# Kernel optimization log

Hardware: AMD Instinct MI355X
Metric: run time of the kernel (lower is better)

Reference implementation:

```python
import jax, jax.numpy as jnp
import numpy as np

N, C_IN, C_OUT, HID, HEADS, K = 8192, 256, 256, 256, 4, 16
DH = HID // HEADS
EPS = 1e-12


def _safe_norm(v, axis=-1):
    return jnp.sqrt(jnp.sum(v * v, axis=axis) + EPS)


def _angle(u, v):
    # angle(u, v) = atan2(||u x v||, u . v)  (standard PPF angle)
    cross = jnp.cross(u, v)
    return jnp.arctan2(_safe_norm(cross), jnp.sum(u * v, axis=-1))


def setup_inputs() -> dict:
    key = jax.random.key(0)
    ks = jax.random.split(key, 12)
    w = lambda k, sh, fan: (jax.random.normal(k, sh, jnp.float32) / np.sqrt(fan)).astype(jnp.float32)
    return {
        'p': jax.random.uniform(ks[0], (N, 3), jnp.float32),
        'normals': jax.random.normal(ks[1], (N, 3), jnp.float32),
        'x': jax.random.normal(ks[2], (N, C_IN), jnp.float32),
        'Wq': w(ks[3], (C_IN, HID), C_IN), 'bq': jnp.zeros((HID,), jnp.float32),
        'Wk': w(ks[4], (C_IN, HID), C_IN), 'bk': jnp.zeros((HID,), jnp.float32),
        'Wv': w(ks[5], (C_IN, HID), C_IN), 'bv': jnp.zeros((HID,), jnp.float32),
        'Wp1': w(ks[6], (4, HID), 4), 'bp1': jnp.zeros((HID,), jnp.float32),
        'Wp2': w(ks[7], (HID, HID), HID), 'bp2': jnp.zeros((HID,), jnp.float32),
        'Wo': w(ks[8], (HID, C_OUT), HID), 'bo': jnp.zeros((C_OUT,), jnp.float32),
    }


def reference(p, normals, x, Wq, bq, Wk, bk, Wv, bv, Wp1, bp1, Wp2, bp2, Wo, bo):
    normals = normals / _safe_norm(normals)[:, None]
    # --- kNN grouping (queryandgroup, stride==1: queries == support) ---
    sq = jnp.sum(p * p, axis=-1)                      # [N]
    d2 = sq[:, None] + sq[None, :] - 2.0 * (p @ p.T)  # [N, N]
    _, group_idx = jax.lax.top_k(-d2, K)              # [N, K] nearest (incl. self)
    c_p = p[group_idx]        # [N, K, 3]
    c_n = normals[group_idx]  # [N, K, 3]
    # --- PPF features (calc_ppf_gpu) ---
    vec_d = c_p - p[:, None, :]                       # [N, K, 3]
    dist = _safe_norm(vec_d)                          # [N, K]
    n1 = jnp.broadcast_to(normals[:, None, :], c_n.shape)
    ppf = jnp.stack([_angle(n1, vec_d), _angle(c_n, vec_d), _angle(n1, c_n), dist], axis=-1)  # [N, K, 4]
    # --- Local PPF transformer: grouped multi-head attention with PPF pos-enc ---
    q = (x @ Wq + bq).reshape(N, HEADS, DH)           # [N, H, Dh]
    feats = x[group_idx]                              # [N, K, C_IN]
    pe = jax.nn.relu(ppf @ Wp1 + bp1) @ Wp2 + bp2     # [N, K, HID]
    kf = (feats @ Wk + bk + pe).reshape(N, K, HEADS, DH)
    vf = (feats @ Wv + bv + pe).reshape(N, K, HEADS, DH)
    logits = jnp.einsum('nhd,nkhd->nhk', q, kf) / np.sqrt(DH)
    attn = jax.nn.softmax(logits, axis=-1)            # [N, H, K]
    out = jnp.einsum('nhk,nkhd->nhd', attn, vf).reshape(N, HID)
    return out @ Wo + bo                              # [N, C_OUT]
```

## Files before the change

### kernel.cpp

```cpp
#include <hip/hip_runtime.h>
#include <math.h>
#include <float.h>

#define NPTS 8192
#define CIN 256
#define HIDN 256
#define KNN 16

typedef unsigned short ushort_t;
typedef unsigned int uint_t;

__device__ __forceinline__ ushort_t f2b(float f) {
  uint_t u = __float_as_uint(f);
  u += 0x7fff + ((u >> 16) & 1);
  return (ushort_t)(u >> 16);
}
__device__ __forceinline__ float b2f(ushort_t s) {
  return __uint_as_float(((uint_t)s) << 16);
}

__global__ __launch_bounds__(256) void prep_kernel(const float* __restrict__ p,
                                                   const float* __restrict__ nr,
                                                   float* __restrict__ sq,
                                                   float* __restrict__ un) {
  int i = blockIdx.x * blockDim.x + threadIdx.x;
  if (i >= NPTS) return;
  float x = p[3*i+0], y = p[3*i+1], z = p[3*i+2];
  sq[i] = x*x + y*y + z*z;
  float a = nr[3*i+0], b = nr[3*i+1], c = nr[3*i+2];
  float nrm = sqrtf(a*a + b*b + c*c + 1e-12f);
  un[3*i+0] = a / nrm;
  un[3*i+1] = b / nrm;
  un[3*i+2] = c / nrm;
}

__device__ __forceinline__ bool dless(float d1, int i1, float d2, int i2) {
  return (d1 < d2) || (d1 == d2 && i1 < i2);
}

__global__ __launch_bounds__(256) void knn_kernel(const float* __restrict__ p,
                                                  const float* __restrict__ sq,
                                                  int* __restrict__ gidx) {
  const int wave = threadIdx.x >> 6;
  const int lane = threadIdx.x & 63;
  const int n = blockIdx.x * 4 + wave;
  const float px = p[3*n+0], py = p[3*n+1], pz = p[3*n+2];
  const float sn = sq[n];
  float d[KNN]; int id[KNN];
#pragma unroll
  for (int i = 0; i < KNN; ++i) { d[i] = FLT_MAX; id[i] = 0x7fffffff; }

  for (int c = 0; c < NPTS/64; ++c) {
    int j = c*64 + lane;
    float ax = p[3*j+0], ay = p[3*j+1], az = p[3*j+2];
    float dot = px*ax + py*ay + pz*az;
    float d2 = sn + sq[j] - 2.0f*dot;
    if (dless(d2, j, d[KNN-1], id[KNN-1])) {
      float cd = d2; int cj = j;
#pragma unroll
      for (int i = 0; i < KNN; ++i) {
        bool b = dless(cd, cj, d[i], id[i]);
        float td = d[i]; int tj = id[i];
        d[i]  = b ? cd : td;  id[i] = b ? cj : tj;
        cd    = b ? td : cd;  cj    = b ? tj : cj;
      }
    }
  }
  for (int r = 0; r < KNN; ++r) {
    float md = d[0]; int mj = id[0];
#pragma unroll
    for (int s = 1; s < 64; s <<= 1) {
      float od = __shfl_xor(md, s);
      int   oj = __shfl_xor(mj, s);
      if (dless(od, oj, md, mj)) { md = od; mj = oj; }
    }
    if (d[0] == md && id[0] == mj) {
#pragma unroll
      for (int i = 0; i < KNN-1; ++i) { d[i] = d[i+1]; id[i] = id[i+1]; }
      d[KNN-1] = FLT_MAX; id[KNN-1] = 0x7fffffff;
    }
    if (lane == 0) gidx[n*KNN + r] = mj;
  }
}

__global__ __launch_bounds__(128) void tile_gemm_kernel(const float* __restrict__ A,
                                                        const float* __restrict__ W,
                                                        const float* __restrict__ bias,
                                                        float* __restrict__ out) {
  __shared__ float At[16][36];
  __shared__ float Bs[16][132];
  const int t = threadIdx.x;
  const int row0 = blockIdx.x * 32;
  const int col0 = blockIdx.y * 128;
  const int tr = t & 7;
  const int tc = t >> 3;
  float acc[4][8];
#pragma unroll
  for (int i = 0; i < 4; ++i)
#pragma unroll
    for (int j = 0; j < 8; ++j) acc[i][j] = 0.f;

  for (int kt = 0; kt < 16; ++kt) {
    __syncthreads();
    {
      const int kk = t & 15, rb = t >> 4;
#pragma unroll
      for (int i = 0; i < 4; ++i) {
        int r = rb*4 + i;
        At[kk][r] = A[(size_t)(row0 + r)*256 + kt*16 + kk];
      }
#pragma unroll
      for (int k = 0; k < 16; ++k)
        Bs[k][t] = W[(size_t)(kt*16 + k)*256 + col0 + t];
    }
    __syncthreads();
#pragma unroll
    for (int k = 0; k < 16; ++k) {
      float4 a4 = *(const float4*)&At[k][tr*4];
      float4 b0 = *(const float4*)&Bs[k][tc*8];
      float4 b1 = *(const float4*)&Bs[k][tc*8 + 4];
      float av[4] = {a4.x, a4.y, a4.z, a4.w};
      float bv[8] = {b0.x, b0.y, b0.z, b0.w, b1.x, b1.y, b1.z, b1.w};
#pragma unroll
      for (int i = 0; i < 4; ++i)
#pragma unroll
        for (int j = 0; j < 8; ++j) acc[i][j] = fmaf(av[i], bv[j], acc[i][j]);
    }
  }
  float4 bb0 = *(const float4*)(bias + col0 + tc*8);
  float4 bb1 = *(const float4*)(bias + col0 + tc*8 + 4);
  float bv[8] = {bb0.x, bb0.y, bb0.z, bb0.w, bb1.x, bb1.y, bb1.z, bb1.w};
#pragma unroll
  for (int i = 0; i < 4; ++i) {
    int row = row0 + tr*4 + i;
    float4 o0, o1;
    o0.x = acc[i][0]+bv[0]; o0.y = acc[i][1]+bv[1]; o0.z = acc[i][2]+bv[2]; o0.w = acc[i][3]+bv[3];
    o1.x = acc[i][4]+bv[4]; o1.y = acc[i][5]+bv[5]; o1.z = acc[i][6]+bv[6]; o1.w = acc[i][7]+bv[7];
    *(float4*)(out + (size_t)row*256 + col0 + tc*8)     = o0;
    *(float4*)(out + (size_t)row*256 + col0 + tc*8 + 4) = o1;
  }
}

__global__ __launch_bounds__(256) void gemmG_kernel(const float* __restrict__ qx,
                                                    const float* __restrict__ Wp2,
                                                    uint_t* __restrict__ G) {
  __shared__ float At[16][68];
  __shared__ float Bs[16][260];
  const int t = threadIdx.x;
  const int row0 = blockIdx.x * 64;
  const int h = blockIdx.y;
  const int tr = t & 15;
  const int tc = t >> 4;
  float acc[4][16];
#pragma unroll
  for (int i = 0; i < 4; ++i)
#pragma unroll
    for (int j = 0; j < 16; ++j) acc[i][j] = 0.f;

  for (int kt = 0; kt < 4; ++kt) {
    __syncthreads();
    {
      const int kk = t & 15, rb = t >> 4;
#pragma unroll
      for (int i = 0; i < 4; ++i) {
        int r = rb*4 + i;
        At[kk][r] = qx[(size_t)(row0 + r)*256 + h*64 + kt*16 + kk];
      }
      const float* src = Wp2 + (size_t)t*256 + h*64 + kt*16;
#pragma unroll
      for (int q = 0; q < 4; ++q) {
        float4 v = *(const float4*)(src + q*4);
        Bs[q*4+0][t] = v.x;
        Bs[q*4+1][t] = v.y;
        Bs[q*4+2][t] = v.z;
        Bs[q*4+3][t] = v.w;
      }
    }
    __syncthreads();
#pragma unroll
    for (int k = 0; k < 16; ++k) {
      float4 a4 = *(const float4*)&At[k][tr*4];
      float av[4] = {a4.x, a4.y, a4.z, a4.w};
#pragma unroll
      for (int q = 0; q < 4; ++q) {
        float4 b4 = *(const float4*)&Bs[k][tc*16 + q*4];
        float bvv[4] = {b4.x, b4.y, b4.z, b4.w};
#pragma unroll
        for (int i = 0; i < 4; ++i)
#pragma unroll
          for (int e = 0; e < 4; ++e)
            acc[i][q*4+e] = fmaf(av[i], bvv[e], acc[i][q*4+e]);
      }
    }
  }
#pragma unroll
  for (int i = 0; i < 4; ++i) {
    int row = row0 + tr*4 + i;
#pragma unroll
    for (int j2 = 0; j2 < 8; ++j2) {
      uint_t pack = ((uint_t)f2b(acc[i][j2*2+1]) << 16) | (uint_t)f2b(acc[i][j2*2]);
      G[(size_t)row*512 + h*128 + tc*8 + j2] = pack;
    }
  }
}

__device__ __forceinline__ float angle3(float ux, float uy, float uz,
                                        float vx, float vy, float vz) {
  float cx = uy*vz - uz*vy;
  float cy = uz*vx - ux*vz;
  float cz = ux*vy - uy*vx;
  float cn = sqrtf(cx*cx + cy*cy + cz*cz + 1e-12f);
  float d  = ux*vx + uy*vy + uz*vz;
  return atan2f(cn, d);
}

__global__ __launch_bounds__(128) void fused_attn2_kernel(
    const float* __restrict__ p, const float* __restrict__ un,
    const int* __restrict__ gidx,
    const float* __restrict__ Wp1, const float* __restrict__ bp1,
    const float* __restrict__ bp2,
    const float* __restrict__ qx, const float* __restrict__ kx,
    const float* __restrict__ vx,
    const ushort_t* __restrict__ G, ushort_t* __restrict__ hbar,
    float* __restrict__ att) {
  __shared__ int   gid_s[KNN];
  __shared__ float ppf_s[KNN][4];
  __shared__ float h1_s[KNN][260];
  __shared__ float G_s[1024];
  __shared__ float q_s[256];
  __shared__ float w_s[64];
  const int n = blockIdx.x;
  const int t = threadIdx.x;

  if (t < KNN) gid_s[t] = gidx[n*KNN + t];
  q_s[t]       = qx[(size_t)n*256 + t];
  q_s[t + 128] = qx[(size_t)n*256 + t + 128];
  {
    const uint_t* gp = (const uint_t*)(G + (size_t)n*1024) + t*4;
#pragma unroll
    for (int q = 0; q < 4; ++q) {
      uint_t raw = gp[q];
      G_s[t*8 + q*2]     = __uint_as_float(raw << 16);
      G_s[t*8 + q*2 + 1] = __uint_as_float(raw & 0xffff0000u);
    }
  }
  __syncthreads();
  if (t < KNN) {
    int g = gid_s[t];
    float dx = p[3*g+0] - p[3*n+0];
    float dy = p[3*g+1] - p[3*n+1];
    float dz = p[3*g+2] - p[3*n+2];
    float n1x = un[3*n+0], n1y = un[3*n+1], n1z = un[3*n+2];
    float n2x = un[3*g+0], n2y = un[3*g+1], n2z = un[3*g+2];
    ppf_s[t][0] = angle3(n1x,n1y,n1z, dx,dy,dz);
    ppf_s[t][1] = angle3(n2x,n2y,n2z, dx,dy,dz);
    ppf_s[t][2] = angle3(n1x,n1y,n1z, n2x,n2y,n2z);
    ppf_s[t][3] = sqrtf(dx*dx + dy*dy + dz*dz + 1e-12f);
  }
  __syncthreads();

  {
    float w0[4], w1[4];
#pragma unroll
    for (int c = 0; c < 4; ++c) {
      w0[c] = Wp1[c*256 + t];
      w1[c] = Wp1[c*256 + t + 128];
    }
    float b0 = bp1[t], b1 = bp1[t+128];
#pragma unroll
    for (int k = 0; k < KNN; ++k) {
      float a0 = ppf_s[k][0], a1 = ppf_s[k][1], a2 = ppf_s[k][2], a3 = ppf_s[k][3];
      float s0 = b0 + a0*w0[0] + a1*w0[1] + a2*w0[2] + a3*w0[3];
      float s1 = b1 + a0*w1[0] + a1*w1[1] + a2*w1[2] + a3*w1[3];
      h1_s[k][t]     = fmaxf(s0, 0.f);
      h1_s[k][t+128] = fmaxf(s1, 0.f);
    }
  }
  __syncthreads();

  {
    const int pr = t >> 1;
    const int h  = pr >> 4;
    const int k  = pr & 15;
    const int half = t & 1;
    const int g = gid_s[k];
    float s = 0.f;
    const float* Gh = G_s + h*256 + half*128;
    const float* H  = &h1_s[k][half*128];
#pragma unroll 8
    for (int j4 = 0; j4 < 32; ++j4) {
      float4 gv = *(const float4*)(Gh + j4*4);
      float4 hv = *(const float4*)(H + j4*4);
      s = fmaf(gv.x, hv.x, s); s = fmaf(gv.y, hv.y, s);
      s = fmaf(gv.z, hv.z, s); s = fmaf(gv.w, hv.w, s);
    }
    const float* qh = q_s + h*64 + half*32;
    const float* kr = kx + (size_t)g*256 + h*64 + half*32;
#pragma unroll
    for (int c4 = 0; c4 < 8; ++c4) {
      float4 qv = *(const float4*)(qh + c4*4);
      float4 kv = *(const float4*)(kr + c4*4);
      s = fmaf(qv.x, kv.x, s); s = fmaf(qv.y, kv.y, s);
      s = fmaf(qv.z, kv.z, s); s = fmaf(qv.w, kv.w, s);
    }
    s += __shfl_xor(s, 1);
    float logit = s * 0.125f;
    float m = logit;
    m = fmaxf(m, __shfl_xor(m, 2));
    m = fmaxf(m, __shfl_xor(m, 4));
    m = fmaxf(m, __shfl_xor(m, 8));
    m = fmaxf(m, __shfl_xor(m, 16));
    float e = expf(logit - m);
    float sum = e;
    sum += __shfl_xor(sum, 2);
    sum += __shfl_xor(sum, 4);
    sum += __shfl_xor(sum, 8);
    sum += __shfl_xor(sum, 16);
    float w = e / sum;
    if (half == 0) w_s[pr] = w;
  }
  __syncthreads();

  {
    float hb0[4] = {0,0,0,0}, hb1[4] = {0,0,0,0};
#pragma unroll
    for (int kk = 0; kk < KNN; ++kk) {
      float h1v0 = h1_s[kk][t];
      float h1v1 = h1_s[kk][t+128];
#pragma unroll
      for (int hh = 0; hh < 4; ++hh) {
        float wv = w_s[hh*16 + kk];
        hb0[hh] = fmaf(wv, h1v0, hb0[hh]);
        hb1[hh] = fmaf(wv, h1v1, hb1[hh]);
      }
    }
#pragma unroll
    for (int hh = 0; hh < 4; ++hh) {
      hbar[(size_t)n*1024 + hh*256 + t]       = f2b(hb0[hh]);
      hbar[(size_t)n*1024 + hh*256 + t + 128] = f2b(hb1[hh]);
    }
  }

  {
    const int h0 = t >> 6;
    const int h1i = 2 + (t >> 6);
    float o0 = bp2[t], o1 = bp2[t+128];
#pragma unroll
    for (int kk = 0; kk < KNN; ++kk) {
      int gg = gid_s[kk];
      float w0v = w_s[h0*16 + kk];
      float w1v = w_s[h1i*16 + kk];
      o0 = fmaf(w0v, vx[(size_t)gg*256 + t], o0);
      o1 = fmaf(w1v, vx[(size_t)gg*256 + t + 128], o1);
    }
    att[(size_t)n*256 + t]       = o0;
    att[(size_t)n*256 + t + 128] = o1;
  }
}

__global__ __launch_bounds__(64) void gemm2_kernel(const ushort_t* __restrict__ hbar,
                                                   const float* __restrict__ Wp2,
                                                   float* __restrict__ att) {
  __shared__ float At[16][68];
  __shared__ float Bs[16][68];
  const int t = threadIdx.x;
  const int row0 = blockIdx.x * 64;
  const int h = blockIdx.y;
  const int tr = t & 7;
  const int tc = t >> 3;
  float acc[8][8];
#pragma unroll
  for (int i = 0; i < 8; ++i)
#pragma unroll
    for (int j = 0; j < 8; ++j) acc[i][j] = 0.f;

  for (int kt = 0; kt < 16; ++kt) {
    __syncthreads();
    {
      const int kk = t & 15, rb = t >> 4;
#pragma unroll
      for (int i = 0; i < 16; ++i) {
        int r = rb*16 + i;
        At[kk][r] = b2f(hbar[(size_t)(row0 + r)*1024 + h*256 + kt*16 + kk]);
      }
#pragma unroll
      for (int k = 0; k < 16; ++k)
        Bs[k][t] = Wp2[(size_t)(kt*16 + k)*256 + h*64 + t];
    }
    __syncthreads();
#pragma unroll
    for (int k = 0; k < 16; ++k) {
      float4 a0 = *(const float4*)&At[k][tr*8];
      float4 a1 = *(const float4*)&At[k][tr*8 + 4];
      float4 b0 = *(const float4*)&Bs[k][tc*8];
      float4 b1 = *(const float4*)&Bs[k][tc*8 + 4];
      float av[8] = {a0.x,a0.y,a0.z,a0.w,a1.x,a1.y,a1.z,a1.w};
      float bv[8] = {b0.x,b0.y,b0.z,b0.w,b1.x,b1.y,b1.z,b1.w};
#pragma unroll
      for (int i = 0; i < 8; ++i)
#pragma unroll
        for (int j = 0; j < 8; ++j) acc[i][j] = fmaf(av[i], bv[j], acc[i][j]);
    }
  }
#pragma unroll
  for (int i = 0; i < 8; ++i) {
    int row = row0 + tr*8 + i;
    float* dst = att + (size_t)row*256 + h*64 + tc*8;
    float4 o0 = *(const float4*)dst;
    float4 o1 = *(const float4*)(dst + 4);
    o0.x += acc[i][0]; o0.y += acc[i][1]; o0.z += acc[i][2]; o0.w += acc[i][3];
    o1.x += acc[i][4]; o1.y += acc[i][5]; o1.z += acc[i][6]; o1.w += acc[i][7];
    *(float4*)dst = o0;
    *(float4*)(dst + 4) = o1;
  }
}

extern "C" void kernel_launch(void* const* d_in, const int* in_sizes, int n_in,
                              void* d_out, int out_size, void* d_ws, size_t ws_size,
                              hipStream_t stream) {
  const float* p   = (const float*)d_in[0];
  const float* nr  = (const float*)d_in[1];
  const float* x   = (const float*)d_in[2];
  const float* Wq  = (const float*)d_in[3];
  const float* bq  = (const float*)d_in[4];
  const float* Wk  = (const float*)d_in[5];
  const float* bk  = (const float*)d_in[6];
  const float* Wv  = (const float*)d_in[7];
  const float* bv  = (const float*)d_in[8];
  const float* Wp1 = (const float*)d_in[9];
  const float* bp1 = (const float*)d_in[10];
  const float* Wp2 = (const float*)d_in[11];
  const float* bp2 = (const float*)d_in[12];
  const float* Wo  = (const float*)d_in[13];
  const float* bo  = (const float*)d_in[14];
  float* out = (float*)d_out;

  float* ws  = (float*)d_ws;
  float* sq  = ws;
  float* un  = sq + NPTS;
  float* qx  = un + (size_t)NPTS*3;
  float* kx  = qx + (size_t)NPTS*HIDN;
  float* vx  = kx + (size_t)NPTS*HIDN;
  float* att = vx + (size_t)NPTS*HIDN;
  int*   gid = (int*)(att + (size_t)NPTS*HIDN);
  ushort_t* G    = (ushort_t*)(gid + (size_t)NPTS*KNN);
  ushort_t* hbar = G + (size_t)NPTS*1024;

  prep_kernel<<<NPTS/256, 256, 0, stream>>>(p, nr, sq, un);
  knn_kernel<<<NPTS/4, 256, 0, stream>>>(p, sq, gid);
  tile_gemm_kernel<<<dim3(NPTS/32, 2), 128, 0, stream>>>(x, Wq, bq, qx);
  tile_gemm_kernel<<<dim3(NPTS/32, 2), 128, 0, stream>>>(x, Wk, bk, kx);
  tile_gemm_kernel<<<dim3(NPTS/32, 2), 128, 0, stream>>>(x, Wv, bv, vx);
  gemmG_kernel<<<dim3(NPTS/64, 4), 256, 0, stream>>>(qx, Wp2, (uint_t*)G);
  fused_attn2_kernel<<<NPTS, 128, 0, stream>>>(p, un, gid, Wp1, bp1, bp2,
                                               qx, kx, vx, G, hbar, att);
  gemm2_kernel<<<dim3(NPTS/64, 4), 64, 0, stream>>>(hbar, Wp2, att);
  tile_gemm_kernel<<<dim3(NPTS/32, 2), 128, 0, stream>>>(att, Wo, bo, out);
}
```

Measured before the change: 519.0 us.

## Merge kNN search and QKV projections into one heterogeneous launch

Replaces the separate kNN kernel and three QKV tile-GEMM launches with a single kernel whose blocks are interleaved, 8 kNN blocks to every 3 GEMM blocks. The compute-heavy GEMM work can then run concurrently with the latency-bound kNN scan, and three launches go away. Each GEMM block now computes two 128-column halves with 256 threads. The cost is doubled shared memory per block and register pressure that is the maximum of both paths, which may reduce occupancy for the kNN blocks.

```diff
diff --git a/kernel.cpp b/kernel.cpp
--- a/kernel.cpp
+++ b/kernel.cpp
@@ -38,48 +38,120 @@
   return (d1 < d2) || (d1 == d2 && i1 < i2);
 }
 
-__global__ __launch_bounds__(256) void knn_kernel(const float* __restrict__ p,
-                                                  const float* __restrict__ sq,
-                                                  int* __restrict__ gidx) {
-  const int wave = threadIdx.x >> 6;
-  const int lane = threadIdx.x & 63;
-  const int n = blockIdx.x * 4 + wave;
-  const float px = p[3*n+0], py = p[3*n+1], pz = p[3*n+2];
-  const float sn = sq[n];
-  float d[KNN]; int id[KNN];
-#pragma unroll
-  for (int i = 0; i < KNN; ++i) { d[i] = FLT_MAX; id[i] = 0x7fffffff; }
-
-  for (int c = 0; c < NPTS/64; ++c) {
-    int j = c*64 + lane;
-    float ax = p[3*j+0], ay = p[3*j+1], az = p[3*j+2];
-    float dot = px*ax + py*ay + pz*az;
-    float d2 = sn + sq[j] - 2.0f*dot;
-    if (dless(d2, j, d[KNN-1], id[KNN-1])) {
-      float cd = d2; int cj = j;
-#pragma unroll
-      for (int i = 0; i < KNN; ++i) {
-        bool b = dless(cd, cj, d[i], id[i]);
-        float td = d[i]; int tj = id[i];
-        d[i]  = b ? cd : td;  id[i] = b ? cj : tj;
-        cd    = b ? td : cd;  cj    = b ? tj : cj;
-      }
-    }
-  }
-  for (int r = 0; r < KNN; ++r) {
-    float md = d[0]; int mj = id[0];
-#pragma unroll
-    for (int s = 1; s < 64; s <<= 1) {
-      float od = __shfl_xor(md, s);
-      int   oj = __shfl_xor(mj, s);
-      if (dless(od, oj, md, mj)) { md = od; mj = oj; }
-    }
-    if (d[0] == md && id[0] == mj) {
-#pragma unroll
-      for (int i = 0; i < KNN-1; ++i) { d[i] = d[i+1]; id[i] = id[i+1]; }
-      d[KNN-1] = FLT_MAX; id[KNN-1] = 0x7fffffff;
-    }
-    if (lane == 0) gidx[n*KNN + r] = mj;
+__global__ __launch_bounds__(256) void knn_qkv_kernel(
+    const float* __restrict__ p, const float* __restrict__ sq,
+    int* __restrict__ gidx,
+    const float* __restrict__ x,
+    const float* __restrict__ Wq, const float* __restrict__ bq,
+    const float* __restrict__ Wk, const float* __restrict__ bk,
+    const float* __restrict__ Wv, const float* __restrict__ bv,
+    float* __restrict__ qx, float* __restrict__ kx, float* __restrict__ vx) {
+  __shared__ float At[2][16][36];
+  __shared__ float Bs[2][16][132];
+  const int L = blockIdx.x;
+  const int grp = L / 11;
+  const int rem = L - grp * 11;
+
+  if (rem < 8) {
+    const int kb = grp * 8 + rem;
+    const int wave = threadIdx.x >> 6;
+    const int lane = threadIdx.x & 63;
+    const int n = kb * 4 + wave;
+    const float px = p[3*n+0], py = p[3*n+1], pz = p[3*n+2];
+    const float sn = sq[n];
+    float d[KNN]; int id[KNN];
+#pragma unroll
+    for (int i = 0; i < KNN; ++i) { d[i] = FLT_MAX; id[i] = 0x7fffffff; }
+
+    for (int c = 0; c < NPTS/64; ++c) {
+      int j = c*64 + lane;
+      float ax = p[3*j+0], ay = p[3*j+1], az = p[3*j+2];
+      float dot = px*ax + py*ay + pz*az;
+      float d2 = sn + sq[j] - 2.0f*dot;
+      if (dless(d2, j, d[KNN-1], id[KNN-1])) {
+        float cd = d2; int cj = j;
+#pragma unroll
+        for (int i = 0; i < KNN; ++i) {
+          bool b = dless(cd, cj, d[i], id[i]);
+          float td = d[i]; int tj = id[i];
+          d[i]  = b ? cd : td;  id[i] = b ? cj : tj;
+          cd    = b ? td : cd;  cj    = b ? tj : cj;
+        }
+      }
+    }
+    for (int r = 0; r < KNN; ++r) {
+      float md = d[0]; int mj = id[0];
+#pragma unroll
+      for (int s = 1; s < 64; s <<= 1) {
+        float od = __shfl_xor(md, s);
+        int   oj = __shfl_xor(mj, s);
+        if (dless(od, oj, md, mj)) { md = od; mj = oj; }
+      }
+      if (d[0] == md && id[0] == mj) {
+#pragma unroll
+        for (int i = 0; i < KNN-1; ++i) { d[i] = d[i+1]; id[i] = id[i+1]; }
+        d[KNN-1] = FLT_MAX; id[KNN-1] = 0x7fffffff;
+      }
+      if (lane == 0) gidx[n*KNN + r] = mj;
+    }
+  } else {
+    const int gb = grp * 3 + (rem - 8);
+    const int w  = gb >> 8;
+    const int rb_ = gb & 255;
+    const float* W    = (w == 0) ? Wq : (w == 1) ? Wk : Wv;
+    const float* bias = (w == 0) ? bq : (w == 1) ? bk : bv;
+    float* out        = (w == 0) ? qx : (w == 1) ? kx : vx;
+    const int g2 = threadIdx.x >> 7;
+    const int t  = threadIdx.x & 127;
+    const int row0 = rb_ * 32;
+    const int col0 = g2 * 128;
+    const int tr = t & 7;
+    const int tc = t >> 3;
+    float acc[4][8];
+#pragma unroll
+    for (int i = 0; i < 4; ++i)
+#pragma unroll
+      for (int j = 0; j < 8; ++j) acc[i][j] = 0.f;
+
+    for (int kt = 0; kt < 16; ++kt) {
+      __syncthreads();
+      {
+        const int kk = t & 15, rb = t >> 4;
+#pragma unroll
+        for (int i = 0; i < 4; ++i) {
+          int r = rb*4 + i;
+          At[g2][kk][r] = x[(size_t)(row0 + r)*256 + kt*16 + kk];
+        }
+#pragma unroll
+        for (int k = 0; k < 16; ++k)
+          Bs[g2][k][t] = W[(size_t)(kt*16 + k)*256 + col0 + t];
+      }
+      __syncthreads();
+#pragma unroll
+      for (int k = 0; k < 16; ++k) {
+        float4 a4 = *(const float4*)&At[g2][k][tr*4];
+        float4 b0 = *(const float4*)&Bs[g2][k][tc*8];
+        float4 b1 = *(const float4*)&Bs[g2][k][tc*8 + 4];
+        float av[4] = {a4.x, a4.y, a4.z, a4.w};
+        float bv8[8] = {b0.x, b0.y, b0.z, b0.w, b1.x, b1.y, b1.z, b1.w};
+#pragma unroll
+        for (int i = 0; i < 4; ++i)
+#pragma unroll
+          for (int j = 0; j < 8; ++j) acc[i][j] = fmaf(av[i], bv8[j], acc[i][j]);
+      }
+    }
+    float4 bb0 = *(const float4*)(bias + col0 + tc*8);
+    float4 bb1 = *(const float4*)(bias + col0 + tc*8 + 4);
+    float bv8[8] = {bb0.x, bb0.y, bb0.z, bb0.w, bb1.x, bb1.y, bb1.z, bb1.w};
+#pragma unroll
+    for (int i = 0; i < 4; ++i) {
+      int row = row0 + tr*4 + i;
+      float4 o0, o1;
+      o0.x = acc[i][0]+bv8[0]; o0.y = acc[i][1]+bv8[1]; o0.z = acc[i][2]+bv8[2]; o0.w = acc[i][3]+bv8[3];
+      o1.x = acc[i][4]+bv8[4]; o1.y = acc[i][5]+bv8[5]; o1.z = acc[i][6]+bv8[6]; o1.w = acc[i][7]+bv8[7];
+      *(float4*)(out + (size_t)row*256 + col0 + tc*8)     = o0;
+      *(float4*)(out + (size_t)row*256 + col0 + tc*8 + 4) = o1;
+    }
   }
 }
 
@@ -447,10 +519,9 @@
   ushort_t* hbar = G + (size_t)NPTS*1024;
 
   prep_kernel<<<NPTS/256, 256, 0, stream>>>(p, nr, sq, un);
-  knn_kernel<<<NPTS/4, 256, 0, stream>>>(p, sq, gid);
-  tile_gemm_kernel<<<dim3(NPTS/32, 2), 128, 0, stream>>>(x, Wq, bq, qx);
-  tile_gemm_kernel<<<dim3(NPTS/32, 2), 128, 0, stream>>>(x, Wk, bk, kx);
-  tile_gemm_kernel<<<dim3(NPTS/32, 2), 128, 0, stream>>>(x, Wv, bv, vx);
+  knn_qkv_kernel<<<2816, 256, 0, stream>>>(p, sq, gid, x,
+                                           Wq, bq, Wk, bk, Wv, bv,
+                                           qx, kx, vx);
   gemmG_kernel<<<dim3(NPTS/64, 4), 256, 0, stream>>>(qx, Wp2, (uint_t*)G);
   fused_attn2_kernel<<<NPTS, 128, 0, stream>>>(p, un, gid, Wp1, bp1, bp2,
                                                qx, kx, vx, G, hbar, att);
```

Result: faster. 495.4 us (-4.5%).
